# Kernel optimization log

Hardware: AMD Instinct MI355X
Metric: run time of the kernel (lower is better)

The kernel has to match this reference:

```python
import jax, jax.numpy as jnp
import numpy as np
from jax import lax

B, C, H, W = 32, 3, 128, 128
S = 10             # max_segments
L = 200            # base_traj_length
TOTAL_LIMIT = 200  # traj_length (must equal L per original sample())
DOF = 2
HID = 2048
CONV_OUT = 512 * 6 * 6  # 128->126->63->61->30->28->14->12->6


def _conv(x, w, b):
    y = lax.conv_general_dilated(x, w, (1, 1), 'VALID', dimension_numbers=('NCHW', 'OIHW', 'NCHW'))
    return y + b[None, :, None, None]


def _pool_relu(x):
    return jax.nn.relu(lax.reduce_window(x, -jnp.inf, lax.max, (1, 1, 2, 2), (1, 1, 2, 2), 'VALID'))


def _rotate2d(y, y0, rot):
    # rotate points y (B,L,2) around per-batch center y0 (B,2) by rot (B,1,1) radians
    px, py = y[..., 0:1], y[..., 1:2]
    cx, cy = y0[:, 0][:, None, None], y0[:, 1][:, None, None]
    c, s = jnp.cos(rot), jnp.sin(rot)
    return jnp.concatenate([c * (px - cx) - s * (py - cy) + cx,
                            s * (px - cx) + c * (py - cy) + cy], axis=2)


def _sample(traj, ratio):
    b, T = traj.shape[0], traj.shape[1]
    f32 = traj.dtype
    seg_limit = jnp.ceil(ratio * TOTAL_LIMIT)  # (B,S)
    # redistribution: shave 1 off the (first) max segment while over budget.
    # original runs over_limit.max() iterations; over_limit <= S-1, extras are no-ops (still_over gate).
    for _ in range(S):
        max_val = seg_limit.max(axis=1)
        still_over = (seg_limit.sum(axis=1) != float(L)).astype(f32)
        reduced = jnp.ones((b,), f32)
        for j in range(S):
            mult = jnp.abs(jnp.sign(max_val - seg_limit[:, j]) - 1.0)
            seg_limit = seg_limit.at[:, j].add(-mult * reduced * still_over)
            reduced = jnp.clip(reduced - mult, 0.0)
    seg_ids = np.arange(T) // L
    # replicates original condition: i>0 and cur_segment_idx != floor(i - 1/L)  (note: i - 1/L, as written)
    forces = np.array([(i > 0) and (seg_ids[i] != int(np.floor(i - 1.0 / L))) for i in range(T)])
    di0 = jnp.floor((L - 1.0) / seg_limit[:, 0:1])
    init = (di0, jnp.zeros((b, 1), f32), jnp.zeros((b, 1), f32), jnp.zeros((b, S), f32))

    def step(state, inp):
        di, last_idx, n_tot, seg_cnt = state
        i_f, seg, force = inp
        lim = lax.dynamic_index_in_dim(seg_limit, seg, axis=1, keepdims=True)  # (B,1)
        cnt = lax.dynamic_index_in_dim(seg_cnt, seg, axis=1, keepdims=True)    # (B,1)
        new_di = jnp.floor((L - 1.0 - (last_idx - seg.astype(f32) * L)) / (lim - cnt))
        di = jnp.where(force | (di < new_di), new_di, di)
        chk = (jnp.sign(jnp.clip(TOTAL_LIMIT - n_tot, 0.0))
               * (cnt < lim).astype(f32)
               * (i_f - last_idx == di).astype(f32))
        last_idx = jnp.maximum(last_idx, i_f * chk)
        seg_cnt = lax.dynamic_update_index_in_dim(seg_cnt, (cnt + chk)[:, 0], seg, axis=1)
        return (di, last_idx, n_tot + chk, seg_cnt), chk[:, 0]

    xs = (jnp.arange(T, dtype=f32), jnp.asarray(seg_ids, jnp.int32), jnp.asarray(forces))
    _, mask_t = lax.scan(step, init, xs)
    mask = mask_t.T > 0  # (B,T) velocity mask; exactly TOTAL_LIMIT true per row
    idx = jnp.argsort(jnp.where(mask, 0, 1), axis=1)[:, :TOTAL_LIMIT]  # stable sort -> ordered true positions
    return jnp.take_along_axis(traj, idx[:, :, None], axis=1)


def _forward(x, w1, b1, w2, b2, w3, b3, w4, b4, fcw1, fcb1, fcw2, fcb2,
             wi, bi, ws, bs, wr, br, base_traj):
    h = _pool_relu(_conv(x, w1, b1))
    h = _pool_relu(_conv(h, w2, b2))
    h = _pool_relu(_conv(h, w3, b3))
    h = _pool_relu(_conv(h, w4, b4))
    feat = h.reshape(h.shape[0], -1)  # (B, CONV_OUT)
    z = jnp.tanh(feat @ fcw1.T + fcb1)
    z = z @ fcw2.T + fcb2             # dropout == identity (eval mode)
    init_pos = z @ wi.T + bi                                   # (B,DOF)
    seg_mod = (z @ ws.T + bs).reshape(z.shape[0], S, DOF + 1)  # (B,S,DOF+1)
    ratio = jax.nn.softmax(z @ wr.T + br, axis=1)              # (B,S)
    last_pos = init_pos[:, None, :]
    starts, segs = [last_pos], []
    for i in range(S):
        scaling = seg_mod[:, i, :-1]
        rot = jnp.tanh(seg_mod[:, i, -1])[:, None, None] * 3.14
        m = base_traj * scaling[:, None, :]
        m = _rotate2d(m, m[:, 0, :], rot)
        m = last_pos + m
        last_pos = m[:, -1:, :]
        starts.append(last_pos)
        segs.append(m)
    traj = jnp.concatenate(segs, axis=1)             # (B,S*L,DOF) unsampled
    seg_start_end = jnp.concatenate(starts, axis=1)  # (B,S+1,DOF)
    sampled = _sample(traj, ratio)                   # (B,TOTAL_LIMIT,DOF)
    return sampled, seg_start_end, ratio, traj


def setup_inputs():
    key = jax.random.key(0)
    ks = jax.random.split(key, 12)
    n = lambda k, s, sc: jax.random.normal(k, s, jnp.float32) * sc
    t = jnp.linspace(0.0, 1.0, L)
    base_traj = jnp.stack([t, jnp.sin(t * jnp.pi)], axis=-1)[None]  # (1,L,2)
    return {
        'x': n(ks[0], (B, C, H, W), 1.0),
        'w1': n(ks[1], (64, C, 3, 3), 0.05), 'b1': jnp.zeros((64,), jnp.float32),
        'w2': n(ks[2], (128, 64, 3, 3), 0.05), 'b2': jnp.zeros((128,), jnp.float32),
        'w3': n(ks[3], (256, 128, 3, 3), 0.05), 'b3': jnp.zeros((256,), jnp.float32),
        'w4': n(ks[4], (512, 256, 3, 3), 0.05), 'b4': jnp.zeros((512,), jnp.float32),
        'fcw1': n(ks[5], (HID, CONV_OUT), 0.01), 'fcb1': jnp.zeros((HID,), jnp.float32),
        'fcw2': n(ks[6], (HID, HID), 0.02), 'fcb2': jnp.zeros((HID,), jnp.float32),
        'wi': n(ks[7], (DOF, HID), 0.02), 'bi': jnp.zeros((DOF,), jnp.float32),
        'ws': n(ks[8], (S * (DOF + 1), HID), 0.02), 'bs': jnp.zeros((S * (DOF + 1),), jnp.float32),
        'wr': n(ks[9], (S, HID), 0.05), 'br': jnp.zeros((S,), jnp.float32),
        'base_traj': base_traj,
    }


def reference(x, w1, b1, w2, b2, w3, b3, w4, b4, fcw1, fcb1, fcw2, fcb2,
              wi, bi, ws, bs, wr, br, base_traj):
    return _forward(x, w1, b1, w2, b2, w3, b3, w4, b4, fcw1, fcb1, fcw2, fcb2,
                    wi, bi, ws, bs, wr, br, base_traj)
```

## Files before the change

### kernel.cpp

```cpp
#include <hip/hip_runtime.h>

__global__ __launch_bounds__(256)
void conv1_lds(const float* __restrict__ in, const float* __restrict__ wt,
               const float* __restrict__ bias, float* __restrict__ out)
{
    __shared__ float sh[3][34][34];
    int bx = blockIdx.x;
    int tile = bx & 15;
    int cg   = (bx >> 4) & 7;
    int b    = bx >> 7;
    int tr = tile >> 2, tc = tile & 3;
    int tid = threadIdx.x;
    int ty = tid >> 4, tx = tid & 15;
    int R0 = 32 * tr, C0 = 32 * tc;

    for (int t = tid; t < 3 * 34 * 34; t += 256) {
        int ci = t / 1156;
        int rem = t - ci * 1156;
        int rr = rem / 34, cc = rem - rr * 34;
        int gr = R0 + rr; if (gr > 127) gr = 127;
        int gc = C0 + cc; if (gc > 127) gc = 127;
        sh[ci][rr][cc] = in[(((size_t)b * 3 + ci) * 128 + gr) * 128 + gc];
    }
    __syncthreads();

    float acc[8][2][2] = {};
    int co0 = cg * 8;
#pragma unroll
    for (int ci = 0; ci < 3; ++ci) {
        float p[4][4];
#pragma unroll
        for (int r = 0; r < 4; ++r) {
            const float2* pr = reinterpret_cast<const float2*>(&sh[ci][2 * ty + r][2 * tx]);
            float2 a = pr[0], c2 = pr[1];
            p[r][0] = a.x; p[r][1] = a.y; p[r][2] = c2.x; p[r][3] = c2.y;
        }
#pragma unroll
        for (int j = 0; j < 8; ++j) {
            const float* wj = wt + ((size_t)(co0 + j) * 3 + ci) * 9;
#pragma unroll
            for (int kh = 0; kh < 3; ++kh)
#pragma unroll
                for (int kw = 0; kw < 3; ++kw) {
                    float wv = wj[kh * 3 + kw];
#pragma unroll
                    for (int dy = 0; dy < 2; ++dy)
#pragma unroll
                        for (int dx = 0; dx < 2; ++dx)
                            acc[j][dy][dx] = fmaf(wv, p[dy + kh][dx + kw], acc[j][dy][dx]);
                }
        }
    }
    int py = 16 * tr + ty, px = 16 * tc + tx;
    if (py < 63 && px < 63) {
#pragma unroll
        for (int j = 0; j < 8; ++j) {
            float v = fmaxf(fmaxf(acc[j][0][0], acc[j][0][1]),
                            fmaxf(acc[j][1][0], acc[j][1][1])) + bias[co0 + j];
            out[(((size_t)b * 64 + co0 + j) * 63 + py) * 63 + px] = fmaxf(v, 0.f);
        }
    }
}

template<int CIN, int DIM, int POOL, int COUT, int TILES_R, int TILES_C>
__global__ __launch_bounds__(256)
void conv_v9(const float* __restrict__ in, const float* __restrict__ wt,
             const float* __restrict__ bias, float* __restrict__ out)
{
    __shared__ __align__(16) float in_sh[2][648];
    __shared__ __align__(16) float w_sh[2][384];

    constexpr int NT  = TILES_R * TILES_C;
    constexpr int NCG = COUT / 32;
    int bx = blockIdx.x;
    int tile = bx % NT;
    int cg   = (bx / NT) % NCG;
    int b    = bx / (NT * NCG);
    int rt = tile / TILES_C, ct = tile % TILES_C;
    int tid = threadIdx.x;
    int co_l = tid & 15;
    int sp   = tid >> 4;
    int ty = sp >> 2, tx = sp & 3;
    int R0 = 16 * rt, C0 = 32 * ct;

    int gofs[3], lofs[3];
#pragma unroll
    for (int j = 0; j < 3; ++j) {
        int t = tid + 256 * j; if (t > 611) t = 611;
        int rr = t / 34, cc = t - rr * 34;
        int gr = R0 + rr; if (gr > DIM - 1) gr = DIM - 1;
        int gc = C0 + cc; if (gc > DIM - 1) gc = DIM - 1;
        gofs[j] = gr * DIM + gc;
        lofs[j] = rr * 36 + cc;
    }
    int wgofs[2], wlofs[2];
#pragma unroll
    for (int j = 0; j < 2; ++j) {
        int t = tid + 256 * j; if (t > 287) t = 287;
        int c = t / 9, k = t - c * 9;
        wgofs[j] = (cg * 32 + c) * CIN * 9 + k;
        wlofs[j] = c * 12 + k;
    }
    bool wv1 = (tid < 32);

    const float* gci = in + (size_t)b * CIN * DIM * DIM;
    const float* wci = wt;

    float acc[2][4][8] = {};
    float sr[3], wr[2];

#pragma unroll
    for (int j = 0; j < 3; ++j) sr[j] = gci[gofs[j]];
    wr[0] = wci[wgofs[0]];
    wr[1] = wci[wgofs[1]];
#pragma unroll
    for (int j = 0; j < 3; ++j) { int t = tid + 256 * j; if (t < 612) in_sh[0][lofs[j]] = sr[j]; }
    w_sh[0][wlofs[0]] = wr[0];
    if (wv1) w_sh[0][wlofs[1]] = wr[1];
    __syncthreads();

    for (int ci = 0; ci < CIN; ++ci) {
        int p = ci & 1;
        if (ci < CIN - 1) {
            const float* gn = gci + (size_t)(ci + 1) * DIM * DIM;
            const float* wn = wci + (size_t)(ci + 1) * 9;
#pragma unroll
            for (int j = 0; j < 3; ++j) sr[j] = gn[gofs[j]];
            wr[0] = wn[wgofs[0]];
            wr[1] = wn[wgofs[1]];
        }
        float w[2][9];
#pragma unroll
        for (int h = 0; h < 2; ++h)
#pragma unroll
            for (int k = 0; k < 9; ++k)
                w[h][k] = w_sh[p][(co_l + 16 * h) * 12 + k];
        const float* rb = in_sh[p] + 8 * tx;
#pragma unroll
        for (int r = 0; r < 6; ++r) {
            const float* rp = rb + (4 * ty + r) * 36;
            float4 a = *reinterpret_cast<const float4*>(rp);
            float4 b4 = *reinterpret_cast<const float4*>(rp + 4);
            float2 c2 = *reinterpret_cast<const float2*>(rp + 8);
            float row[10];
            row[0] = a.x;  row[1] = a.y;  row[2] = a.z;  row[3] = a.w;
            row[4] = b4.x; row[5] = b4.y; row[6] = b4.z; row[7] = b4.w;
            row[8] = c2.x; row[9] = c2.y;
#pragma unroll
            for (int y = 0; y < 4; ++y) {
                if (y < r - 2 || y > r) continue;
                int kh = r - y;
#pragma unroll
                for (int kw = 0; kw < 3; ++kw) {
                    float w0 = w[0][kh * 3 + kw];
                    float w1 = w[1][kh * 3 + kw];
#pragma unroll
                    for (int x = 0; x < 8; ++x) {
                        acc[0][y][x] = fmaf(w0, row[x + kw], acc[0][y][x]);
                        acc[1][y][x] = fmaf(w1, row[x + kw], acc[1][y][x]);
                    }
                }
            }
        }
        if (ci < CIN - 1) {
#pragma unroll
            for (int j = 0; j < 3; ++j) { int t = tid + 256 * j; if (t < 612) in_sh[p ^ 1][lofs[j]] = sr[j]; }
            w_sh[p ^ 1][wlofs[0]] = wr[0];
            if (wv1) w_sh[p ^ 1][wlofs[1]] = wr[1];
        }
        __syncthreads();
    }

#pragma unroll
    for (int h = 0; h < 2; ++h) {
        int co = cg * 32 + co_l + 16 * h;
        float bz = bias[co];
#pragma unroll
        for (int dy = 0; dy < 2; ++dy) {
            int py = 8 * rt + 2 * ty + dy;
#pragma unroll
            for (int dx = 0; dx < 4; ++dx) {
                int px = 16 * ct + 4 * tx + dx;
                if (py < POOL && px < POOL) {
                    float v = fmaxf(fmaxf(acc[h][2 * dy][2 * dx],     acc[h][2 * dy][2 * dx + 1]),
                                    fmaxf(acc[h][2 * dy + 1][2 * dx], acc[h][2 * dy + 1][2 * dx + 1]));
                    out[(((size_t)b * COUT + co) * POOL + py) * POOL + px] = fmaxf(v + bz, 0.f);
                }
            }
        }
    }
}

__global__ __launch_bounds__(256)
void conv3_v10(const float* __restrict__ in, const float* __restrict__ wt,
               const float* __restrict__ bias, float* __restrict__ out)
{
    __shared__ __align__(16) float in_sh[2][360];
    __shared__ __align__(16) float w_sh[2][384];

    int bx = blockIdx.x;
    int tile = bx & 3;
    int cg   = (bx >> 2) & 7;
    int b    = bx >> 5;
    int rt = tile >> 1, ct = tile & 1;
    int tid = threadIdx.x;
    int co_l = tid & 15;
    int sp   = tid >> 4;
    int ty = sp >> 2, tx = sp & 3;
    int R0 = 16 * rt, C0 = 16 * ct;

    int gofs[2];
#pragma unroll
    for (int j = 0; j < 2; ++j) {
        int t = tid + 256 * j; if (t > 359) t = 359;
        int rr = t / 20, cc = t - rr * 20;
        int gr = R0 + rr; if (gr > 29) gr = 29;
        int gc = C0 + cc; if (gc > 29) gc = 29;
        gofs[j] = gr * 30 + gc;
    }
    int lo1 = (tid + 256 > 359) ? 359 : tid + 256;
    int wgofs[2], wlofs[2];
#pragma unroll
    for (int j = 0; j < 2; ++j) {
        int t = tid + 256 * j; if (t > 287) t = 287;
        int c = t / 9, k = t - c * 9;
        wgofs[j] = (cg * 32 + c) * 128 * 9 + k;
        wlofs[j] = c * 12 + k;
    }
    bool wv1 = (tid < 32);

    const float* gci = in + (size_t)b * 128 * 900;
    const float* wci = wt;

    float acc[2][4][4] = {};
    float sr[2], wr[2];

    sr[0] = gci[gofs[0]];
    sr[1] = gci[gofs[1]];
    wr[0] = wci[wgofs[0]];
    wr[1] = wci[wgofs[1]];
    in_sh[0][tid] = sr[0];
    if (tid < 104) in_sh[0][lo1] = sr[1];
    w_sh[0][wlofs[0]] = wr[0];
    if (wv1) w_sh[0][wlofs[1]] = wr[1];
    __syncthreads();

    for (int ci = 0; ci < 128; ++ci) {
        int p = ci & 1;
        if (ci < 127) {
            const float* gn = gci + (size_t)(ci + 1) * 900;
            const float* wn = wci + (size_t)(ci + 1) * 9;
            sr[0] = gn[gofs[0]];
            sr[1] = gn[gofs[1]];
            wr[0] = wn[wgofs[0]];
            wr[1] = wn[wgofs[1]];
        }
        float w[2][9];
#pragma unroll
        for (int h = 0; h < 2; ++h)
#pragma unroll
            for (int k = 0; k < 9; ++k)
                w[h][k] = w_sh[p][(co_l + 16 * h) * 12 + k];
        const float* rb = in_sh[p] + 4 * tx;
#pragma unroll
        for (int r = 0; r < 6; ++r) {
            const float* rp = rb + (4 * ty + r) * 20;
            float4 a = *reinterpret_cast<const float4*>(rp);
            float2 c2 = *reinterpret_cast<const float2*>(rp + 4);
            float row[6];
            row[0] = a.x; row[1] = a.y; row[2] = a.z; row[3] = a.w;
            row[4] = c2.x; row[5] = c2.y;
#pragma unroll
            for (int y = 0; y < 4; ++y) {
                if (y < r - 2 || y > r) continue;
                int kh = r - y;
#pragma unroll
                for (int kw = 0; kw < 3; ++kw) {
                    float w0 = w[0][kh * 3 + kw];
                    float w1 = w[1][kh * 3 + kw];
#pragma unroll
                    for (int x = 0; x < 4; ++x) {
                        acc[0][y][x] = fmaf(w0, row[x + kw], acc[0][y][x]);
                        acc[1][y][x] = fmaf(w1, row[x + kw], acc[1][y][x]);
                    }
                }
            }
        }
        if (ci < 127) {
            in_sh[p ^ 1][tid] = sr[0];
            if (tid < 104) in_sh[p ^ 1][lo1] = sr[1];
            w_sh[p ^ 1][wlofs[0]] = wr[0];
            if (wv1) w_sh[p ^ 1][wlofs[1]] = wr[1];
        }
        __syncthreads();
    }

#pragma unroll
    for (int h = 0; h < 2; ++h) {
        int co = cg * 32 + co_l + 16 * h;
        float bz = bias[co];
#pragma unroll
        for (int dy = 0; dy < 2; ++dy) {
            int py = 8 * rt + 2 * ty + dy;
#pragma unroll
            for (int dx = 0; dx < 2; ++dx) {
                int px = 8 * ct + 2 * tx + dx;
                if (py < 14 && px < 14) {
                    float v = fmaxf(fmaxf(acc[h][2 * dy][2 * dx],     acc[h][2 * dy][2 * dx + 1]),
                                    fmaxf(acc[h][2 * dy + 1][2 * dx], acc[h][2 * dy + 1][2 * dx + 1]));
                    out[(((size_t)b * 256 + co) * 14 + py) * 14 + px] = fmaxf(v + bz, 0.f);
                }
            }
        }
    }
}

__global__ __launch_bounds__(256)
void conv4_v3(const float* __restrict__ in, const float* __restrict__ wt,
              const float* __restrict__ bias, float* __restrict__ out)
{
    __shared__ __align__(16) float smem[4032 + 4 * 16 * 37];
    float* in_sh = smem;
    float* w_sh  = smem + 4032;
    float* red   = smem;

    int bx = blockIdx.x;
    int cg = bx & 31;
    int b  = bx >> 5;
    int tid = threadIdx.x;
    int h   = tid >> 6;
    int r6  = tid & 63;
    int cog = r6 >> 3;
    int sub = r6 & 7;
    int R = 3 * (sub >> 1), C = 6 * (sub & 1);

    float acc[2][3][6] = {};
    float sin_r[13];
    float sw_r[9];

    const size_t in_b = (size_t)b * 256 * 196;

#pragma unroll
    for (int j = 0; j < 13; ++j) {
        int g = tid + 256 * j;
        if (g < 3136) {
            int hh = g / 784, rem = g - hh * 784;
            int ci = rem / 196, r2 = rem - ci * 196;
            sin_r[j] = in[in_b + (size_t)(hh * 64 + ci) * 196 + r2];
        }
    }
#pragma unroll
    for (int j = 0; j < 9; ++j) {
        int g = tid + 256 * j;
        int hh = g / 576, rem = g - hh * 576;
        int co = rem / 36, q = rem - co * 36;
        sw_r[j] = wt[(size_t)(cg * 16 + co) * 2304 + (size_t)(hh * 64) * 9 + q];
    }

    for (int it = 0; it < 16; ++it) {
#pragma unroll
        for (int j = 0; j < 13; ++j) {
            int g = tid + 256 * j;
            if (g < 3136) {
                int hh = g / 784, rem = g - hh * 784;
                int ci = rem / 196, r2 = rem - ci * 196;
                int rr = r2 / 14, cc = r2 - rr * 14;
                in_sh[((hh * 4 + ci) * 14 + rr) * 18 + cc] = sin_r[j];
            }
        }
#pragma unroll
        for (int j = 0; j < 9; ++j) {
            int g = tid + 256 * j;
            int hh = g / 576, rem = g - hh * 576;
            int co = rem / 36, q = rem - co * 36;
            w_sh[(hh * 16 + co) * 37 + q] = sw_r[j];
        }
        __syncthreads();
        if (it < 15) {
            int k0n = (it + 1) * 4;
#pragma unroll
            for (int j = 0; j < 13; ++j) {
                int g = tid + 256 * j;
                if (g < 3136) {
                    int hh = g / 784, rem = g - hh * 784;
                    int ci = rem / 196, r2 = rem - ci * 196;
                    sin_r[j] = in[in_b + (size_t)(hh * 64 + k0n + ci) * 196 + r2];
                }
            }
#pragma unroll
            for (int j = 0; j < 9; ++j) {
                int g = tid + 256 * j;
                int hh = g / 576, rem = g - hh * 576;
                int co = rem / 36, q = rem - co * 36;
                sw_r[j] = wt[(size_t)(cg * 16 + co) * 2304 + (size_t)(hh * 64 + k0n) * 9 + q];
            }
        }
#pragma unroll
        for (int ci = 0; ci < 4; ++ci) {
            float w[2][9];
#pragma unroll
            for (int c = 0; c < 2; ++c)
#pragma unroll
                for (int k = 0; k < 9; ++k)
                    w[c][k] = w_sh[(h * 16 + 2 * cog + c) * 37 + ci * 9 + k];
            const float* rowbase = in_sh + ((h * 4 + ci) * 14) * 18;
#pragma unroll
            for (int r = 0; r < 5; ++r) {
                float row[8];
                const float2* pr = reinterpret_cast<const float2*>(rowbase + (size_t)(R + r) * 18 + C);
                float2 a0 = pr[0], a1 = pr[1], a2 = pr[2], a3 = pr[3];
                row[0] = a0.x; row[1] = a0.y; row[2] = a1.x; row[3] = a1.y;
                row[4] = a2.x; row[5] = a2.y; row[6] = a3.x; row[7] = a3.y;
#pragma unroll
                for (int y = 0; y < 3; ++y) {
                    if (y < r - 2 || y > r) continue;
                    int kh = r - y;
#pragma unroll
                    for (int c = 0; c < 2; ++c)
#pragma unroll
                        for (int kw = 0; kw < 3; ++kw) {
                            float wv = w[c][kh * 3 + kw];
#pragma unroll
                            for (int x = 0; x < 6; ++x)
                                acc[c][y][x] = fmaf(wv, row[x + kw], acc[c][y][x]);
                        }
                }
            }
        }
        __syncthreads();
    }
#pragma unroll
    for (int hh = 0; hh < 4; ++hh) {
        if (h == hh) {
#pragma unroll
            for (int c = 0; c < 2; ++c)
#pragma unroll
                for (int y = 0; y < 3; ++y)
#pragma unroll
                    for (int x = 0; x < 6; ++x) {
                        float* dst = &red[((2 * cog + c) * 12 + R + y) * 13 + C + x];
                        if (hh == 0) *dst = acc[c][y][x];
                        else         *dst += acc[c][y][x];
                    }
        }
        __syncthreads();
    }
    for (int t = tid; t < 576; t += 256) {
        int co = t / 36, rem = t - co * 36;
        int pr = rem / 6, pc = rem - pr * 6;
        const float* rp = &red[(co * 12 + 2 * pr) * 13 + 2 * pc];
        float v = fmaxf(fmaxf(rp[0], rp[1]), fmaxf(rp[13], rp[14]));
        v += bias[cg * 16 + co];
        out[(((size_t)b * 512 + cg * 16 + co) * 6 + pr) * 6 + pc] = fmaxf(v, 0.f);
    }
}

__global__ __launch_bounds__(1024)
void fc_big(const float* __restrict__ X, const float* __restrict__ W,
            const float* __restrict__ bias, float* __restrict__ Y,
            int K, int N, int act)
{
    __shared__ float red[32][32][8];
    int o0 = blockIdx.x * 8;
    int s = threadIdx.x & 31;
    int b = threadIdx.x >> 5;
    int K4 = K >> 2;
    const float4* X4 = reinterpret_cast<const float4*>(X) + (size_t)b * K4;
    const float4* W4 = reinterpret_cast<const float4*>(W);

    float acc[8] = {};
    for (int k4 = s; k4 < K4; k4 += 32) {
        float4 xv = X4[k4];
#pragma unroll
        for (int o = 0; o < 8; ++o) {
            float4 wv = W4[(size_t)(o0 + o) * K4 + k4];
            acc[o] = fmaf(xv.x, wv.x,
                     fmaf(xv.y, wv.y,
                     fmaf(xv.z, wv.z,
                     fmaf(xv.w, wv.w, acc[o]))));
        }
    }
#pragma unroll
    for (int o = 0; o < 8; ++o) red[b][s][o] = acc[o];
    __syncthreads();
    if (threadIdx.x < 256) {
        int bb = threadIdx.x >> 3, oo = threadIdx.x & 7;
        float v = bias[o0 + oo];
#pragma unroll 8
        for (int ss = 0; ss < 32; ++ss) v += red[bb][ss][oo];
        if (act) v = tanhf(v);
        Y[(size_t)bb * N + o0 + oo] = v;
    }
}

__global__ __launch_bounds__(256)
void fc_two(const float* __restrict__ X, const float* __restrict__ W,
            const float* __restrict__ bias, float* __restrict__ Y,
            int K, int N, int act)
{
    int o0 = blockIdx.x * 2;
    int tid = threadIdx.x;
    const float* w0 = W + (size_t)o0 * K;
    const float* w1 = w0 + K;
    float a0[32], a1[32];
#pragma unroll
    for (int b = 0; b < 32; ++b) { a0[b] = 0.f; a1[b] = 0.f; }

    for (int k = tid; k < K; k += 256) {
        float wv0 = w0[k], wv1 = w1[k];
#pragma unroll
        for (int b = 0; b < 32; ++b) {
            float xv = X[(size_t)b * K + k];
            a0[b] = fmaf(wv0, xv, a0[b]);
            a1[b] = fmaf(wv1, xv, a1[b]);
        }
    }
    __shared__ float part[2][4][32];
    int lane = tid & 63, wv = tid >> 6;
#pragma unroll
    for (int b = 0; b < 32; ++b) {
        float s0 = a0[b], s1 = a1[b];
#pragma unroll
        for (int off = 32; off >= 1; off >>= 1) {
            s0 += __shfl_down(s0, off);
            s1 += __shfl_down(s1, off);
        }
        if (lane == 0) { part[0][wv][b] = s0; part[1][wv][b] = s1; }
    }
    __syncthreads();
    if (tid < 64) {
        int j = tid >> 5, b = tid & 31;
        float s = part[j][0][b] + part[j][1][b] + part[j][2][b] + part[j][3][b] + bias[o0 + j];
        if (act) s = tanhf(s);
        Y[(size_t)b * N + o0 + j] = s;
    }
}

__global__ __launch_bounds__(64)
void post_kernel(const float* __restrict__ logits, float* __restrict__ ratio_out,
                 float* __restrict__ sl_out)
{
    int b = threadIdx.x;
    if (b >= 32) return;
    float lg[10];
#pragma unroll
    for (int j = 0; j < 10; ++j) lg[j] = logits[b * 10 + j];
    float mx = lg[0];
#pragma unroll
    for (int j = 1; j < 10; ++j) mx = fmaxf(mx, lg[j]);
    float e[10]; float ssum = 0.f;
#pragma unroll
    for (int j = 0; j < 10; ++j) { e[j] = expf(lg[j] - mx); ssum += e[j]; }
    float sl[10];
#pragma unroll
    for (int j = 0; j < 10; ++j) {
        float r = e[j] / ssum;
        ratio_out[b * 10 + j] = r;
        sl[j] = ceilf(r * 200.f);
    }
#pragma unroll
    for (int it = 0; it < 10; ++it) {
        float s = 0.f, mx2 = sl[0];
#pragma unroll
        for (int j = 0; j < 10; ++j) { s += sl[j]; mx2 = fmaxf(mx2, sl[j]); }
        float over = (s != 200.f) ? 1.f : 0.f;
        float reduced = 1.f;
#pragma unroll
        for (int j = 0; j < 10; ++j) {
            float mult = (sl[j] == mx2) ? 1.f : 0.f;
            sl[j] -= mult * reduced * over;
            reduced = fmaxf(reduced - mult, 0.f);
        }
    }
#pragma unroll
    for (int j = 0; j < 10; ++j) sl_out[b * 10 + j] = sl[j];
}

__global__ __launch_bounds__(256)
void traj_kernel(const float* __restrict__ base, const float* __restrict__ ipos,
                 const float* __restrict__ sm, float* __restrict__ out_traj,
                 float* __restrict__ out_starts)
{
    int b = blockIdx.x;
    int j = threadIdx.x;
    float bx0 = base[0], by0 = base[1];
    float bxL = base[398], byL = base[399];
    float bx = 0.f, by = 0.f;
    if (j < 200) { bx = base[2 * j]; by = base[2 * j + 1]; }
    float curx = ipos[b * 2 + 0], cury = ipos[b * 2 + 1];
    if (j == 0) { out_starts[b * 22 + 0] = curx; out_starts[b * 22 + 1] = cury; }
#pragma unroll
    for (int i = 0; i < 10; ++i) {
        float sx  = sm[b * 30 + i * 3 + 0];
        float sy  = sm[b * 30 + i * 3 + 1];
        float rot = tanhf(sm[b * 30 + i * 3 + 2]) * 3.14f;
        float c = cosf(rot), s = sinf(rot);
        float cx = bx0 * sx, cy = by0 * sy;
        if (j < 200) {
            float px = bx * sx, py = by * sy;
            float rx = c * (px - cx) - s * (py - cy) + cx;
            float ry = s * (px - cx) + c * (py - cy) + cy;
            size_t o = ((size_t)b * 2000 + i * 200 + j) * 2;
            out_traj[o + 0] = curx + rx;
            out_traj[o + 1] = cury + ry;
        }
        float pxL = bxL * sx, pyL = byL * sy;
        float exL = c * (pxL - cx) - s * (pyL - cy) + cx;
        float eyL = s * (pxL - cx) + c * (pyL - cy) + cy;
        curx += exL; cury += eyL;
        if (j == 0) {
            out_starts[b * 22 + (i + 1) * 2 + 0] = curx;
            out_starts[b * 22 + (i + 1) * 2 + 1] = cury;
        }
    }
}

__global__ __launch_bounds__(64)
void sample_kernel(const float* __restrict__ sl_in, const float* __restrict__ traj,
                   float* __restrict__ samp_out)
{
    __shared__ unsigned int maskb[32][63];
    __shared__ float ssl[32][10];
    int tid = threadIdx.x;
    for (int t = tid; t < 32 * 63; t += 64) ((unsigned int*)maskb)[t] = 0u;
    for (int t = tid; t < 32 * 10; t += 64) ((float*)ssl)[t] = sl_in[t];
    __syncthreads();
    if (tid >= 32) return;
    int b = tid;
    const float* tb = traj + (size_t)b * 4000;
    float* sp = samp_out + (size_t)b * 400;
    int out_n = 0;
    float last = 0.f, ntot = 0.f;
    float lim0 = ssl[b][0];
    float di = floorf(199.f / lim0);
    float ct0 = 0.f;
    if ((ntot < 200.f) && (ct0 < lim0) && (0.f - last == di)) {
        ntot += 1.f; ct0 += 1.f;
        maskb[b][0] |= 1u;
        sp[out_n * 2] = tb[0]; sp[out_n * 2 + 1] = tb[1]; ++out_n;
    }
    {
        float ndi = floorf((199.f - last) / (lim0 - ct0));
        if (di < ndi) di = ndi;
        if ((ntot < 200.f) && (ct0 < lim0) && (1.f - last == di)) {
            last = 1.f; ntot += 1.f; ct0 += 1.f;
            maskb[b][0] |= 2u;
            sp[out_n * 2] = tb[2]; sp[out_n * 2 + 1] = tb[3]; ++out_n;
        }
    }
    for (int seg = 0; seg < 10; ++seg) {
        float lim = ssl[b][seg];
        float ct = (seg == 0) ? ct0 : 0.f;
        float segbase = 200.f * seg;
        float segend = segbase + 199.f;
        float pos = (seg == 0) ? 2.f : segbase;
        float ndi = floorf((199.f - (last - segbase)) / (lim - ct));
        while ((ntot < 200.f) && (ct < lim)) {
            float fi = last + ndi;
            if (!(fi >= pos && fi <= segend)) break;
            int i = (int)fi;
            last = fi; ntot += 1.f; ct += 1.f;
            maskb[b][i >> 5] |= (1u << (i & 31));
            sp[out_n * 2] = tb[2 * i]; sp[out_n * 2 + 1] = tb[2 * i + 1]; ++out_n;
            pos = fi + 1.f;
            ndi = floorf((199.f - (last - segbase)) / (lim - ct));
        }
    }
    for (int i = 0; i < 2000 && out_n < 200; ++i) {
        if (!((maskb[b][i >> 5] >> (i & 31)) & 1u)) {
            sp[out_n * 2] = tb[2 * i]; sp[out_n * 2 + 1] = tb[2 * i + 1]; ++out_n;
        }
    }
}

extern "C" void kernel_launch(void* const* d_in, const int* in_sizes, int n_in,
                              void* d_out, int out_size, void* d_ws, size_t ws_size,
                              hipStream_t stream)
{
    const float* x    = (const float*)d_in[0];
    const float* w1   = (const float*)d_in[1];
    const float* b1   = (const float*)d_in[2];
    const float* w2   = (const float*)d_in[3];
    const float* b2   = (const float*)d_in[4];
    const float* w3   = (const float*)d_in[5];
    const float* b3   = (const float*)d_in[6];
    const float* w4   = (const float*)d_in[7];
    const float* b4   = (const float*)d_in[8];
    const float* fcw1 = (const float*)d_in[9];
    const float* fcb1 = (const float*)d_in[10];
    const float* fcw2 = (const float*)d_in[11];
    const float* fcb2 = (const float*)d_in[12];
    const float* wi   = (const float*)d_in[13];
    const float* bi   = (const float*)d_in[14];
    const float* wsw  = (const float*)d_in[15];
    const float* bs   = (const float*)d_in[16];
    const float* wr   = (const float*)d_in[17];
    const float* br   = (const float*)d_in[18];
    const float* base = (const float*)d_in[19];

    float* out = (float*)d_out;
    float* ws  = (float*)d_ws;

    float* p1   = ws + 0;
    float* p2   = ws + 8128512;
    float* p3   = ws + 0;
    float* feat = ws + 8128512;
    float* z1   = ws + 0;
    float* z2   = ws + 65536;
    float* ipos = ws + 131072;
    float* smod = ws + 131136;
    float* rlog = ws + 132096;
    float* slim = ws + 132416;

    float* out_samp   = out;
    float* out_starts = out + 12800;
    float* out_ratio  = out + 13504;
    float* out_traj   = out + 13824;

    conv1_lds<<<4096, 256, 0, stream>>>(x, w1, b1, p1);
    conv_v9<64, 63, 30, 128, 4, 2><<<1024, 256, 0, stream>>>(p1, w2, b2, p2);
    conv3_v10<<<1024, 256, 0, stream>>>(p2, w3, b3, p3);
    conv4_v3<<<1024, 256, 0, stream>>>(p3, w4, b4, feat);

    fc_big<<<256, 1024, 0, stream>>>(feat, fcw1, fcb1, z1, 18432, 2048, 1);
    fc_big<<<256, 1024, 0, stream>>>(z1, fcw2, fcb2, z2, 2048, 2048, 0);

    fc_two<<<1, 256, 0, stream>>>(z2, wi, bi, ipos, 2048, 2, 0);
    fc_two<<<15, 256, 0, stream>>>(z2, wsw, bs, smod, 2048, 30, 0);
    fc_two<<<5, 256, 0, stream>>>(z2, wr, br, rlog, 2048, 10, 0);

    post_kernel<<<1, 64, 0, stream>>>(rlog, out_ratio, slim);
    traj_kernel<<<32, 256, 0, stream>>>(base, ipos, smod, out_traj, out_starts);
    sample_kernel<<<1, 64, 0, stream>>>(slim, out_traj, out_samp);
}
```

Before: 1.001 ms.

## Split conv3 input channels across blocks with atomic accumulation and separate pool

conv3 now uses wider tiles (two row-halves covering all columns, 8 output columns per thread) and splits the 128 input channels into two halves processed by separate blocks. Partial pre-pool maps are combined with atomicAdd into a zeroed 28x28 buffer, and a new pool3 kernel applies 2x2 max-pool, bias and ReLU. This raises the register tile size for more FMA per LDS load and shortens the serial channel loop. The cost is a memset, atomics on about 6.4M floats, an extra pass over a full-resolution map, and larger per-thread register use.

```diff
diff --git a/kernel.cpp b/kernel.cpp
--- a/kernel.cpp
+++ b/kernel.cpp
@@ -192,66 +192,68 @@
 }
 
 __global__ __launch_bounds__(256)
-void conv3_v10(const float* __restrict__ in, const float* __restrict__ wt,
-               const float* __restrict__ bias, float* __restrict__ out)
-{
-    __shared__ __align__(16) float in_sh[2][360];
+void conv3_part(const float* __restrict__ in, const float* __restrict__ wt,
+                float* __restrict__ cmap)
+{
+    __shared__ __align__(16) float in_sh[2][648];
     __shared__ __align__(16) float w_sh[2][384];
 
     int bx = blockIdx.x;
-    int tile = bx & 3;
-    int cg   = (bx >> 2) & 7;
-    int b    = bx >> 5;
-    int rt = tile >> 1, ct = tile & 1;
+    int half = bx >> 9;
+    int bxl  = bx & 511;
+    int tile = bxl & 1;
+    int cg   = (bxl >> 1) & 7;
+    int b    = bxl >> 4;
+    int rt = tile;
     int tid = threadIdx.x;
     int co_l = tid & 15;
     int sp   = tid >> 4;
     int ty = sp >> 2, tx = sp & 3;
-    int R0 = 16 * rt, C0 = 16 * ct;
-
-    int gofs[2];
-#pragma unroll
-    for (int j = 0; j < 2; ++j) {
-        int t = tid + 256 * j; if (t > 359) t = 359;
-        int rr = t / 20, cc = t - rr * 20;
+    int R0 = 16 * rt;
+
+    int gofs[3], lofs[3];
+#pragma unroll
+    for (int j = 0; j < 3; ++j) {
+        int t = tid + 256 * j; if (t > 611) t = 611;
+        int rr = t / 34, cc = t - rr * 34;
         int gr = R0 + rr; if (gr > 29) gr = 29;
-        int gc = C0 + cc; if (gc > 29) gc = 29;
+        int gc = cc;      if (gc > 29) gc = 29;
         gofs[j] = gr * 30 + gc;
-    }
-    int lo1 = (tid + 256 > 359) ? 359 : tid + 256;
+        lofs[j] = rr * 36 + cc;
+    }
     int wgofs[2], wlofs[2];
 #pragma unroll
     for (int j = 0; j < 2; ++j) {
         int t = tid + 256 * j; if (t > 287) t = 287;
         int c = t / 9, k = t - c * 9;
-        wgofs[j] = (cg * 32 + c) * 128 * 9 + k;
+        wgofs[j] = (cg * 32 + c) * 128 * 9 + half * 64 * 9 + k;
         wlofs[j] = c * 12 + k;
     }
     bool wv1 = (tid < 32);
 
-    const float* gci = in + (size_t)b * 128 * 900;
+    const float* gci = in + (size_t)b * 128 * 900 + (size_t)half * 64 * 900;
     const float* wci = wt;
 
-    float acc[2][4][4] = {};
-    float sr[2], wr[2];
-
-    sr[0] = gci[gofs[0]];
-    sr[1] = gci[gofs[1]];
+    float acc[2][4][8] = {};
+    float sr[3], wr[2];
+
+#pragma unroll
+    for (int j = 0; j < 3; ++j) sr[j] = gci[gofs[j]];
     wr[0] = wci[wgofs[0]];
     wr[1] = wci[wgofs[1]];
-    in_sh[0][tid] = sr[0];
-    if (tid < 104) in_sh[0][lo1] = sr[1];
+#pragma unroll
+    for (int j = 0; j < 3; ++j) { int t = tid + 256 * j; if (t < 612) in_sh[0][lofs[j]] = sr[j]; }
     w_sh[0][wlofs[0]] = wr[0];
     if (wv1) w_sh[0][wlofs[1]] = wr[1];
     __syncthreads();
 
-    for (int ci = 0; ci < 128; ++ci) {
+    for (int ci = 0; ci < 64; ++ci) {
         int p = ci & 1;
-        if (ci < 127) {
+        if (ci < 63) {
             const float* gn = gci + (size_t)(ci + 1) * 900;
             const float* wn = wci + (size_t)(ci + 1) * 9;
-            sr[0] = gn[gofs[0]];
-            sr[1] = gn[gofs[1]];
+#pragma unroll
+            for (int j = 0; j < 3; ++j) sr[j] = gn[gofs[j]];
             wr[0] = wn[wgofs[0]];
             wr[1] = wn[wgofs[1]];
         }
@@ -261,15 +263,17 @@
 #pragma unroll
             for (int k = 0; k < 9; ++k)
                 w[h][k] = w_sh[p][(co_l + 16 * h) * 12 + k];
-        const float* rb = in_sh[p] + 4 * tx;
+        const float* rb = in_sh[p] + 8 * tx;
 #pragma unroll
         for (int r = 0; r < 6; ++r) {
-            const float* rp = rb + (4 * ty + r) * 20;
+            const float* rp = rb + (4 * ty + r) * 36;
             float4 a = *reinterpret_cast<const float4*>(rp);
-            float2 c2 = *reinterpret_cast<const float2*>(rp + 4);
-            float row[6];
-            row[0] = a.x; row[1] = a.y; row[2] = a.z; row[3] = a.w;
-            row[4] = c2.x; row[5] = c2.y;
+            float4 b4 = *reinterpret_cast<const float4*>(rp + 4);
+            float2 c2 = *reinterpret_cast<const float2*>(rp + 8);
+            float row[10];
+            row[0] = a.x;  row[1] = a.y;  row[2] = a.z;  row[3] = a.w;
+            row[4] = b4.x; row[5] = b4.y; row[6] = b4.z; row[7] = b4.w;
+            row[8] = c2.x; row[9] = c2.y;
 #pragma unroll
             for (int y = 0; y < 4; ++y) {
                 if (y < r - 2 || y > r) continue;
@@ -279,16 +283,16 @@
                     float w0 = w[0][kh * 3 + kw];
                     float w1 = w[1][kh * 3 + kw];
 #pragma unroll
-                    for (int x = 0; x < 4; ++x) {
+                    for (int x = 0; x < 8; ++x) {
                         acc[0][y][x] = fmaf(w0, row[x + kw], acc[0][y][x]);
                         acc[1][y][x] = fmaf(w1, row[x + kw], acc[1][y][x]);
                     }
                 }
             }
         }
-        if (ci < 127) {
-            in_sh[p ^ 1][tid] = sr[0];
-            if (tid < 104) in_sh[p ^ 1][lo1] = sr[1];
+        if (ci < 63) {
+#pragma unroll
+            for (int j = 0; j < 3; ++j) { int t = tid + 256 * j; if (t < 612) in_sh[p ^ 1][lofs[j]] = sr[j]; }
             w_sh[p ^ 1][wlofs[0]] = wr[0];
             if (wv1) w_sh[p ^ 1][wlofs[1]] = wr[1];
         }
@@ -298,21 +302,33 @@
 #pragma unroll
     for (int h = 0; h < 2; ++h) {
         int co = cg * 32 + co_l + 16 * h;
-        float bz = bias[co];
-#pragma unroll
-        for (int dy = 0; dy < 2; ++dy) {
-            int py = 8 * rt + 2 * ty + dy;
-#pragma unroll
-            for (int dx = 0; dx < 2; ++dx) {
-                int px = 8 * ct + 2 * tx + dx;
-                if (py < 14 && px < 14) {
-                    float v = fmaxf(fmaxf(acc[h][2 * dy][2 * dx],     acc[h][2 * dy][2 * dx + 1]),
-                                    fmaxf(acc[h][2 * dy + 1][2 * dx], acc[h][2 * dy + 1][2 * dx + 1]));
-                    out[(((size_t)b * 256 + co) * 14 + py) * 14 + px] = fmaxf(v + bz, 0.f);
-                }
+        float* cb = cmap + ((size_t)b * 256 + co) * 784;
+#pragma unroll
+        for (int y = 0; y < 4; ++y) {
+            int gr = R0 + 4 * ty + y;
+#pragma unroll
+            for (int x = 0; x < 8; ++x) {
+                int gc = 8 * tx + x;
+                if (gr < 28 && gc < 28)
+                    atomicAdd(&cb[gr * 28 + gc], acc[h][y][x]);
             }
         }
     }
+}
+
+__global__ __launch_bounds__(256)
+void pool3(const float* __restrict__ cmap, const float* __restrict__ bias,
+           float* __restrict__ out)
+{
+    int i = blockIdx.x * 256 + threadIdx.x;
+    if (i >= 32 * 256 * 196) return;
+    int px = i % 14;
+    int py = (i / 14) % 14;
+    int co = (i / 196) % 256;
+    int b  = i / 50176;
+    const float* p = cmap + (((size_t)b * 256 + co) * 28 + 2 * py) * 28 + 2 * px;
+    float v = fmaxf(fmaxf(p[0], p[1]), fmaxf(p[28], p[29])) + bias[co];
+    out[i] = fmaxf(v, 0.f);
 }
 
 __global__ __launch_bounds__(256)
@@ -703,7 +719,8 @@
 
     float* p1   = ws + 0;
     float* p2   = ws + 8128512;
-    float* p3   = ws + 0;
+    float* cmap = ws + 0;
+    float* p3   = ws + 6422528;
     float* feat = ws + 8128512;
     float* z1   = ws + 0;
     float* z2   = ws + 65536;
@@ -719,7 +736,11 @@
 
     conv1_lds<<<4096, 256, 0, stream>>>(x, w1, b1, p1);
     conv_v9<64, 63, 30, 128, 4, 2><<<1024, 256, 0, stream>>>(p1, w2, b2, p2);
-    conv3_v10<<<1024, 256, 0, stream>>>(p2, w3, b3, p3);
+
+    hipMemsetAsync(cmap, 0, (size_t)6422528 * sizeof(float), stream);
+    conv3_part<<<1024, 256, 0, stream>>>(p2, w3, cmap);
+    pool3<<<6272, 256, 0, stream>>>(cmap, b3, p3);
+
     conv4_v3<<<1024, 256, 0, stream>>>(p3, w4, b4, feat);
 
     fc_big<<<256, 1024, 0, stream>>>(feat, fcw1, fcb1, z1, 18432, 2048, 1);
```

After: 1.314 ms. +31.2%, slower.
